# Performance work log

Measured on AMD Instinct MI355X. Metric: run time of the kernel, lower is better.

The kernel has to match this reference:

```python
import jax, jax.numpy as jnp
import numpy as np

B, C, N, H, S = 2048, 64, 64, 8, 4
D = C // H          # head dim 8
CS = C // S         # per-scale channels 16
CP = C // 4         # pattern memory dim 16


def _conv1d(x, w, b):
    # x: [B, Cin, N], w: [Cout, Cin, 3], 'same' padding
    y = jax.lax.conv_general_dilated(x, w, (1,), ((1, 1),),
                                     dimension_numbers=('NCH', 'OIH', 'NCH'))
    return y + b[None, :, None]


def setup_inputs() -> dict:
    key = jax.random.key(0)
    ks = jax.random.split(key, 20)
    s = 0.05
    f32 = jnp.float32
    return {
        'x': jax.random.normal(ks[0], (B, C, N), f32),
        'points': jax.random.normal(ks[1], (N, 3), f32),
        'conv1_w': jax.random.normal(ks[2], (S, CS, C, 3), f32) * s,
        'conv1_b': jnp.zeros((S, CS), f32),
        'conv2_w': jax.random.normal(ks[3], (S, CS, CS, 3), f32) * s,
        'conv2_b': jnp.zeros((S, CS), f32),
        'pattern_memory': jax.random.normal(ks[4], (64, CP), f32),
        'pm1_w': jax.random.normal(ks[5], (C, C + CP), f32) * s,
        'pm1_b': jnp.zeros((C,), f32),
        'pm2_w': jax.random.normal(ks[6], (C, C), f32) * s,
        'pm2_b': jnp.zeros((C,), f32),
        'q_w': jax.random.normal(ks[7], (C, C), f32) * s,
        'q_b': jnp.zeros((C,), f32),
        'k_w': jax.random.normal(ks[8], (C, C), f32) * s,
        'k_b': jnp.zeros((C,), f32),
        'v_w': jax.random.normal(ks[9], (C, C), f32) * s,
        'v_b': jnp.zeros((C,), f32),
        'in_w': jax.random.normal(ks[10], (3 * C, C), f32) * s,
        'in_b': jnp.zeros((3 * C,), f32),
        'mo_w': jax.random.normal(ks[11], (C, C), f32) * s,
        'mo_b': jnp.zeros((C,), f32),
        'out_w': jax.random.normal(ks[12], (C, C), f32) * s,
        'out_b': jnp.zeros((C,), f32),
        'ln_g': jnp.ones((C,), f32),
        'ln_beta': jnp.zeros((C,), f32),
        'adjacency': jax.random.randint(ks[13], (64, 64), 0, 2, jnp.int32),
    }


def _forward(x, points, conv1_w, conv1_b, conv2_w, conv2_b, pattern_memory,
             pm1_w, pm1_b, pm2_w, pm2_b, q_w, q_b, k_w, k_b, v_w, v_b,
             in_w, in_b, mo_w, mo_b, out_w, out_b, ln_g, ln_beta, adjacency):
    b, c, n = x.shape
    # multi-scale conv stacks (fixed small loop over scales)
    feats = []
    for i in range(S):
        y = jax.nn.relu(_conv1d(x, conv1_w[i], conv1_b[i]))
        y = jax.nn.relu(_conv1d(y, conv2_w[i], conv2_b[i]))
        feats.append(jnp.transpose(y, (0, 2, 1)))  # [B, N, CS]
    combined = jnp.concatenate(feats, axis=-1)     # [B, N, C]
    # pattern memory broadcast per point (N == 64)
    pat = jnp.broadcast_to(pattern_memory[None], (b, n, CP))
    pi = jnp.concatenate([combined, pat], axis=-1)  # [B, N, C+CP]
    pf = jax.nn.relu(pi @ pm1_w.T + pm1_b) @ pm2_w.T + pm2_b  # [B, N, C]
    q = pf @ q_w.T + q_b
    k = pf @ k_w.T + k_b
    v = pf @ v_w.T + v_b
    # nn.MultiheadAttention: internal in_proj + out_proj
    wq, wk, wv = in_w[:C], in_w[C:2 * C], in_w[2 * C:]
    bq, bk, bv = in_b[:C], in_b[C:2 * C], in_b[2 * C:]
    q2 = (q @ wq.T + bq).reshape(b, n, H, D)
    k2 = (k @ wk.T + bk).reshape(b, n, H, D)
    v2 = (v @ wv.T + bv).reshape(b, n, H, D)
    scale = 1.0 / np.sqrt(D).astype(np.float32)
    scores = jnp.einsum('bnhd,bmhd->bhnm', q2, k2) * scale
    attn = jax.nn.softmax(scores, axis=-1)
    ctx = jnp.einsum('bhnm,bmhd->bnhd', attn, v2).reshape(b, n, C)
    attended = ctx @ mo_w.T + mo_b
    # vectorized geometric bias (replaces the 64x64 python loop)
    diff = points[:, None, :] - points[None, :, :]
    dist = jnp.sqrt(jnp.sum(diff * diff, axis=-1) + 1e-12)
    geo = jnp.where(adjacency > 0, jnp.float32(0.5), -0.1 / (1.0 + dist))
    attended = attended + geo[None]
    # layer norm over channels, then output projection
    h = attended + pf
    mu = jnp.mean(h, axis=-1, keepdims=True)
    var = jnp.mean((h - mu) ** 2, axis=-1, keepdims=True)
    hn = (h - mu) * jax.lax.rsqrt(var + 1e-5) * ln_g + ln_beta
    out = hn @ out_w.T + out_b
    return jnp.transpose(out, (0, 2, 1))  # [B, C, N]


def reference(x, points, conv1_w, conv1_b, conv2_w, conv2_b, pattern_memory,
              pm1_w, pm1_b, pm2_w, pm2_b, q_w, q_b, k_w, k_b, v_w, v_b,
              in_w, in_b, mo_w, mo_b, out_w, out_b, ln_g, ln_beta, adjacency):
    return _forward(x, points, conv1_w, conv1_b, conv2_w, conv2_b,
                    pattern_memory, pm1_w, pm1_b, pm2_w, pm2_b, q_w, q_b,
                    k_w, k_b, v_w, v_b, in_w, in_b, mo_w, mo_b, out_w, out_b,
                    ln_g, ln_beta, adjacency)
```

## Files before the change

### kernel.cpp

```cpp
#include <hip/hip_runtime.h>
#include <math.h>

using bf16x8 = __attribute__((ext_vector_type(8))) __bf16;
using f32x4  = __attribute__((ext_vector_type(4))) float;

#if __has_builtin(__builtin_amdgcn_exp2f)
#define EXP2F(x) __builtin_amdgcn_exp2f(x)
#else
#define EXP2F(x) exp2f(x)
#endif

__device__ __forceinline__ unsigned short f2bf(float f) {
  unsigned u = __float_as_uint(f);
  unsigned r = u + 0x7fffu + ((u >> 16) & 1u);
  return (unsigned short)(r >> 16);
}

__device__ __forceinline__ unsigned cvt_pk_bf16(float a, float b) {
  unsigned r;
  asm("v_cvt_pk_bf16_f32 %0, %1, %2" : "=v"(r) : "v"(a), "v"(b));
  return r;
}
__device__ __forceinline__ uint2 pk4(float a, float b, float c, float d) {
  uint2 r; r.x = cvt_pk_bf16(a, b); r.y = cvt_pk_bf16(c, d); return r;
}

__device__ __forceinline__ f32x4 mfma16(uint4 a, uint4 b, f32x4 c) {
  return __builtin_amdgcn_mfma_f32_16x16x32_bf16(
      __builtin_bit_cast(bf16x8, a), __builtin_bit_cast(bf16x8, b), c, 0, 0, 0);
}
__device__ __forceinline__ float swz_xor16(float v) {
  return __int_as_float(__builtin_amdgcn_ds_swizzle(__float_as_int(v), 0x401F));
}

#define FRAG_OFF(k, n) (((((n) >> 4) * 2 + ((k) >> 5)) * 64 + (((k) >> 3) & 3) * 16 + ((n) & 15)) * 8 + ((k) & 7))

#define ATT_C 0.51006997f

__global__ void precompute_kernel(
    const float* __restrict__ conv1_w, const float* __restrict__ conv2_w,
    const float* __restrict__ pm1_w, const float* __restrict__ pm1_b,
    const float* __restrict__ pm2_w,
    const float* __restrict__ q_w, const float* __restrict__ q_b,
    const float* __restrict__ k_w, const float* __restrict__ k_b,
    const float* __restrict__ v_w, const float* __restrict__ v_b,
    const float* __restrict__ in_w, const float* __restrict__ in_b,
    const float* __restrict__ mo_w, const float* __restrict__ out_w,
    const float* __restrict__ pattern, const float* __restrict__ points,
    const int* __restrict__ adjacency,
    unsigned short* __restrict__ wsb, float* __restrict__ wsf) {
  int idx = blockIdx.x * 256 + threadIdx.x;
  if (idx < 12288) {
    int t = idx >> 12, rem = idx & 4095;
    int oc = rem >> 6, c = rem & 63;
    wsb[idx] = f2bf(conv1_w[(oc * 64 + c) * 3 + t]);
  } else if (idx < 24576) {
    int i2 = idx - 12288;
    int t = i2 >> 12, rem = i2 & 4095;
    int oc = rem >> 6, ci = rem & 63;
    float v = ((ci >> 4) == (oc >> 4)) ? conv2_w[(oc * 16 + (ci & 15)) * 3 + t] : 0.0f;
    wsb[idx] = f2bf(v);
  } else if (idx < 28672) {
    int rem = idx - 24576;
    wsb[idx] = f2bf(pm1_w[(rem >> 6) * 80 + (rem & 63)]);
  } else if (idx < 32768) {
    wsb[idx] = f2bf(pm2_w[idx - 28672]);
  } else if (idx < 36864) {
    int rem = idx - 32768; int c = rem >> 6, k = rem & 63;
    float s = 0.f;
    #pragma unroll 8
    for (int j = 0; j < 64; ++j) s += in_w[c * 64 + j] * q_w[j * 64 + k];
    wsb[idx] = f2bf(s * ATT_C);
  } else if (idx < 40960) {
    int rem = idx - 36864; int c = rem >> 6, k = rem & 63;
    float s = 0.f;
    #pragma unroll 8
    for (int j = 0; j < 64; ++j) s += in_w[(64 + c) * 64 + j] * k_w[j * 64 + k];
    wsb[idx] = f2bf(s);
  } else if (idx < 45056) {
    int rem = idx - 40960; int c = rem >> 6, k = rem & 63;
    float s = 0.f;
    #pragma unroll 8
    for (int j = 0; j < 64; ++j) s += in_w[(128 + c) * 64 + j] * v_w[j * 64 + k];
    wsb[idx] = f2bf(s);
  } else if (idx < 49152) {
    wsb[idx] = f2bf(mo_w[idx - 45056]);
  } else if (idx < 53248) {
    wsb[idx] = f2bf(out_w[idx - 49152]);
  } else if (idx < 57344) {
    int rem = idx - 53248; int c = rem >> 6, n = rem & 63;
    float s = pm1_b[c];
    #pragma unroll
    for (int cp = 0; cp < 16; ++cp) s += pm1_w[c * 80 + 64 + cp] * pattern[n * 16 + cp];
    wsf[rem] = s;
  } else if (idx < 61440) {
    int rem = idx - 57344; int c = rem >> 6, n = rem & 63;
    float dd = 1e-12f;
    #pragma unroll
    for (int i = 0; i < 3; ++i) { float d = points[n * 3 + i] - points[c * 3 + i]; dd += d * d; }
    float dist = sqrtf(dd);
    wsf[4096 + rem] = (adjacency[n * 64 + c] > 0) ? 0.5f : (-0.1f / (1.0f + dist));
  } else if (idx < 61632) {
    int rem = idx - 61440; int which = rem >> 6, c = rem & 63;
    if (which == 0) {
      float s = in_b[c];
      for (int j = 0; j < 64; ++j) s += in_w[c * 64 + j] * q_b[j];
      wsf[8192 + c] = s * ATT_C;
    } else if (which == 1) {
      float s = in_b[64 + c];
      for (int j = 0; j < 64; ++j) s += in_w[(64 + c) * 64 + j] * k_b[j];
      wsf[8256 + c] = s;
    } else {
      float s = in_b[128 + c];
      for (int j = 0; j < 64; ++j) s += in_w[(128 + c) * 64 + j] * v_b[j];
      wsf[8320 + c] = s;
    }
  }
}

__device__ __forceinline__ void gemm64(const unsigned short* __restrict__ Wg,
                                       const unsigned short* Bf,
                                       int wm, int wn, int lane, f32x4 acc[2]) {
  const int l15 = lane & 15, lq = lane >> 4;
  #pragma unroll
  for (int s = 0; s < 2; ++s) {
    bf16x8 a = *reinterpret_cast<const bf16x8*>(Wg + (16 * wm + l15) * 64 + s * 32 + lq * 8);
    #pragma unroll
    for (int nti = 0; nti < 2; ++nti) {
      int nt = 2 * wn + nti;
      bf16x8 bb = *reinterpret_cast<const bf16x8*>(Bf + ((nt * 2 + s) * 64 + lane) * 8);
      acc[nti] = __builtin_amdgcn_mfma_f32_16x16x32_bf16(a, bb, acc[nti], 0, 0, 0);
    }
  }
}

#define SLOT_B 4096
#define KBASE  8704
#define VBASE  13312
#define H32F   2048
#define LNS    6656

__global__ __launch_bounds__(512, 8) void fused_kernel(
    const float* __restrict__ x,
    const unsigned short* __restrict__ wsb, const float* __restrict__ wsf,
    const float* __restrict__ conv1_b, const float* __restrict__ conv2_b,
    const float* __restrict__ pm2_b, const float* __restrict__ mo_b,
    const float* __restrict__ out_b, const float* __restrict__ ln_g,
    const float* __restrict__ ln_beta, float* __restrict__ out) {
  __shared__ __align__(16) unsigned char smem_raw[35840];
  unsigned short* S16 = reinterpret_cast<unsigned short*>(smem_raw);
  float* S32 = reinterpret_cast<float*>(smem_raw);

  const int tid = threadIdx.x;
  const int b = blockIdx.x;
  const int lane = tid & 63;
  const int w = tid >> 6;
  const int wm = w >> 1;
  const int wn = w & 1;
  const int l15 = lane & 15;
  const int lq = lane >> 4;
  const int c0 = 16 * wm + lq * 4;
  f32x4 pfs[2];

  if (tid < 8) S16[VBASE + tid] = 0;
  {
    const float* xb = x + b * 4096 + w * 8 * 64 + lane;
    float v[8];
    #pragma unroll
    for (int j = 0; j < 8; ++j) v[j] = xb[j * 64];
    uint4 u;
    u.x = cvt_pk_bf16(v[0], v[1]);
    u.y = cvt_pk_bf16(v[2], v[3]);
    u.z = cvt_pk_bf16(v[4], v[5]);
    u.w = cvt_pk_bf16(v[6], v[7]);
    *reinterpret_cast<uint4*>(S16 + FRAG_OFF(w * 8, lane)) = u;
  }
  __syncthreads();

  auto conv_pass = [&](const unsigned short* Wg, int srcBase, f32x4 acc[2]) {
    bf16x8 a6[3][2];
    #pragma unroll
    for (int t = 0; t < 3; ++t)
      #pragma unroll
      for (int s = 0; s < 2; ++s)
        a6[t][s] = *reinterpret_cast<const bf16x8*>(Wg + t * 4096 + (16 * wm + l15) * 64 + s * 32 + lq * 8);
    #pragma unroll
    for (int nti = 0; nti < 2; ++nti) {
      int nt = 2 * wn + nti;
      #pragma unroll
      for (int t = 0; t < 3; ++t) {
        int np = nt * 16 + l15 + (t - 1);
        bool ok = (unsigned)np < 64u;
        int a = srcBase + (((np >> 4) * 2) * 64 + lq * 16 + (np & 15)) * 8;
        int A0 = ok ? a : VBASE;
        int A1 = ok ? (a + 512) : VBASE;
        bf16x8 b0 = *reinterpret_cast<const bf16x8*>(S16 + A0);
        bf16x8 b1 = *reinterpret_cast<const bf16x8*>(S16 + A1);
        acc[nti] = __builtin_amdgcn_mfma_f32_16x16x32_bf16(a6[t][0], b0, acc[nti], 0, 0, 0);
        acc[nti] = __builtin_amdgcn_mfma_f32_16x16x32_bf16(a6[t][1], b1, acc[nti], 0, 0, 0);
      }
    }
  };

  {
    f32x4 acc[2] = {};
    conv_pass(wsb, 0, acc);
    float bia[4] = {conv1_b[c0], conv1_b[c0 + 1], conv1_b[c0 + 2], conv1_b[c0 + 3]};
    #pragma unroll
    for (int nti = 0; nti < 2; ++nti) {
      int n = (2 * wn + nti) * 16 + l15;
      uint2 u = pk4(fmaxf(acc[nti][0] + bia[0], 0.f), fmaxf(acc[nti][1] + bia[1], 0.f),
                    fmaxf(acc[nti][2] + bia[2], 0.f), fmaxf(acc[nti][3] + bia[3], 0.f));
      *reinterpret_cast<uint2*>(S16 + SLOT_B + FRAG_OFF(c0, n)) = u;
    }
  }
  __syncthreads();

  {
    f32x4 acc[2] = {};
    conv_pass(wsb + 12288, SLOT_B, acc);
    float bia[4] = {conv2_b[c0], conv2_b[c0 + 1], conv2_b[c0 + 2], conv2_b[c0 + 3]};
    #pragma unroll
    for (int nti = 0; nti < 2; ++nti) {
      int n = (2 * wn + nti) * 16 + l15;
      uint2 u = pk4(fmaxf(acc[nti][0] + bia[0], 0.f), fmaxf(acc[nti][1] + bia[1], 0.f),
                    fmaxf(acc[nti][2] + bia[2], 0.f), fmaxf(acc[nti][3] + bia[3], 0.f));
      *reinterpret_cast<uint2*>(S16 + FRAG_OFF(c0, n)) = u;
    }
  }
  __syncthreads();

  {
    f32x4 acc[2] = {};
    gemm64(wsb + 24576, S16, wm, wn, lane, acc);
    #pragma unroll
    for (int nti = 0; nti < 2; ++nti) {
      int n = (2 * wn + nti) * 16 + l15;
      uint2 u = pk4(fmaxf(acc[nti][0] + wsf[(c0 + 0) * 64 + n], 0.f),
                    fmaxf(acc[nti][1] + wsf[(c0 + 1) * 64 + n], 0.f),
                    fmaxf(acc[nti][2] + wsf[(c0 + 2) * 64 + n], 0.f),
                    fmaxf(acc[nti][3] + wsf[(c0 + 3) * 64 + n], 0.f));
      *reinterpret_cast<uint2*>(S16 + SLOT_B + FRAG_OFF(c0, n)) = u;
    }
  }
  __syncthreads();

  {
    f32x4 acc[2] = {};
    gemm64(wsb + 28672, S16 + SLOT_B, wm, wn, lane, acc);
    float bia[4] = {pm2_b[c0], pm2_b[c0 + 1], pm2_b[c0 + 2], pm2_b[c0 + 3]};
    #pragma unroll
    for (int nti = 0; nti < 2; ++nti) {
      int n = (2 * wn + nti) * 16 + l15;
      f32x4 v;
      #pragma unroll
      for (int r = 0; r < 4; ++r) v[r] = acc[nti][r] + bia[r];
      pfs[nti] = v;
      *reinterpret_cast<uint2*>(S16 + FRAG_OFF(c0, n)) = pk4(v[0], v[1], v[2], v[3]);
    }
  }
  __syncthreads();

  {
    f32x4 acc[2] = {};
    gemm64(wsb + 32768, S16, wm, wn, lane, acc);
    #pragma unroll
    for (int nti = 0; nti < 2; ++nti) {
      int n = (2 * wn + nti) * 16 + l15;
      *reinterpret_cast<uint2*>(S16 + SLOT_B + n * 72 + c0) =
          pk4(acc[nti][0] + wsf[8192 + c0], acc[nti][1] + wsf[8192 + c0 + 1],
              acc[nti][2] + wsf[8192 + c0 + 2], acc[nti][3] + wsf[8192 + c0 + 3]);
    }
  }
  {
    f32x4 acc[2] = {};
    gemm64(wsb + 36864, S16, wm, wn, lane, acc);
    #pragma unroll
    for (int nti = 0; nti < 2; ++nti) {
      int n = (2 * wn + nti) * 16 + l15;
      *reinterpret_cast<uint2*>(S16 + KBASE + n * 72 + c0) =
          pk4(acc[nti][0] + wsf[8256 + c0], acc[nti][1] + wsf[8256 + c0 + 1],
              acc[nti][2] + wsf[8256 + c0 + 2], acc[nti][3] + wsf[8256 + c0 + 3]);
    }
  }
  {
    f32x4 acc[2] = {};
    gemm64(wsb + 40960, S16, wm, wn, lane, acc);
    #pragma unroll
    for (int nti = 0; nti < 2; ++nti) {
      int n = (2 * wn + nti) * 16 + l15;
      #pragma unroll
      for (int r = 0; r < 4; ++r)
        S16[VBASE + (c0 + r) * 72 + n] = f2bf(acc[nti][r] + wsf[8320 + c0 + r]);
    }
  }
  __syncthreads();

  {
    const int h = w;
    const bool lq0 = (lq == 0);
    uint4 vb[2];
    #pragma unroll
    for (int ks = 0; ks < 2; ++ks)
      vb[ks] = *reinterpret_cast<const uint4*>(
          S16 + VBASE + (h * 8 + (l15 & 7)) * 72 + ks * 32 + lq * 8);
    uint4 ka[4];
    #pragma unroll
    for (int mt = 0; mt < 4; ++mt) {
      uint4 t = *reinterpret_cast<const uint4*>(S16 + KBASE + (mt * 16 + l15) * 72 + h * 8);
      ka[mt].x = lq0 ? t.x : 0u; ka[mt].y = lq0 ? t.y : 0u;
      ka[mt].z = lq0 ? t.z : 0u; ka[mt].w = lq0 ? t.w : 0u;
    }
    __syncthreads();

    const int Pb = KBASE + w * 1152;
    #pragma unroll
    for (int q = 0; q < 4; ++q) {
      uint4 qb = *reinterpret_cast<const uint4*>(S16 + SLOT_B + (q * 16 + l15) * 72 + h * 8);
      qb.x = lq0 ? qb.x : 0u; qb.y = lq0 ? qb.y : 0u;
      qb.z = lq0 ? qb.z : 0u; qb.w = lq0 ? qb.w : 0u;
      f32x4 sc[4];
      #pragma unroll
      for (int mt = 0; mt < 4; ++mt) {
        f32x4 z = {0.f, 0.f, 0.f, 0.f};
        sc[mt] = mfma16(ka[mt], qb, z);
      }
      float sum = 0.f;
      #pragma unroll
      for (int mt = 0; mt < 4; ++mt)
        #pragma unroll
        for (int r = 0; r < 4; ++r) {
          float e = EXP2F(sc[mt][r]);
          sc[mt][r] = e; sum += e;
        }
      sum += swz_xor16(sum);
      sum += __shfl_xor(sum, 32);
      float inv = __builtin_amdgcn_rcpf(sum);
      #pragma unroll
      for (int mt = 0; mt < 4; ++mt) {
        unsigned d0 = __builtin_amdgcn_perm(__float_as_uint(sc[mt][1] * inv),
                                            __float_as_uint(sc[mt][0] * inv), 0x07060302u);
        unsigned d1 = __builtin_amdgcn_perm(__float_as_uint(sc[mt][3] * inv),
                                            __float_as_uint(sc[mt][2] * inv), 0x07060302u);
        *reinterpret_cast<uint2*>(S16 + Pb + l15 * 72 + mt * 16 + lq * 4) = make_uint2(d0, d1);
      }
      f32x4 ctx = {0.f, 0.f, 0.f, 0.f};
      #pragma unroll
      for (int ks = 0; ks < 2; ++ks) {
        uint4 pa = *reinterpret_cast<const uint4*>(S16 + Pb + l15 * 72 + ks * 32 + lq * 8);
        ctx = mfma16(pa, vb[ks], ctx);
      }
      if (l15 < 8) {
        const int kk = h * 8 + l15;
        #pragma unroll
        for (int r = 0; r < 4; ++r)
          S16[FRAG_OFF(kk, q * 16 + lq * 4 + r)] = f2bf(ctx[r]);
      }
    }
  }
  __syncthreads();

  {
    f32x4 acc[2] = {};
    gemm64(wsb + 45056, S16, wm, wn, lane, acc);
    #pragma unroll
    for (int nti = 0; nti < 2; ++nti) {
      int n = (2 * wn + nti) * 16 + l15;
      #pragma unroll
      for (int r = 0; r < 4; ++r) {
        int c = c0 + r;
        S32[H32F + c * 65 + n] = acc[nti][r] + mo_b[c] + wsf[4096 + c * 64 + n] + pfs[nti][r];
      }
    }
  }
  __syncthreads();

  {
    int n = tid & 63, qq = tid >> 6;
    float sum = 0.f, ssq = 0.f;
    #pragma unroll
    for (int j = 0; j < 8; ++j) {
      float v = S32[H32F + (qq * 8 + j) * 65 + n];
      sum += v; ssq += v * v;
    }
    S32[LNS + tid] = sum;
    S32[LNS + 512 + tid] = ssq;
    __syncthreads();
    if (tid < 64) {
      float s = 0.f, ss = 0.f;
      #pragma unroll
      for (int i = 0; i < 8; ++i) {
        s  += S32[LNS + i * 64 + tid];
        ss += S32[LNS + 512 + i * 64 + tid];
      }
      float mu = s * (1.0f / 64.0f);
      float var = ss * (1.0f / 64.0f) - mu * mu;
      S32[LNS + 1024 + tid] = mu;
      S32[LNS + 1088 + tid] = rsqrtf(var + 1e-5f);
    }
    __syncthreads();
    float mu = S32[LNS + 1024 + n], rs = S32[LNS + 1088 + n];
    int ch0 = qq * 8;
    float vv[8];
    #pragma unroll
    for (int jj = 0; jj < 8; ++jj) {
      int c = ch0 + jj;
      vv[jj] = (S32[H32F + c * 65 + n] - mu) * rs * ln_g[c] + ln_beta[c];
    }
    uint4 u;
    u.x = cvt_pk_bf16(vv[0], vv[1]);
    u.y = cvt_pk_bf16(vv[2], vv[3]);
    u.z = cvt_pk_bf16(vv[4], vv[5]);
    u.w = cvt_pk_bf16(vv[6], vv[7]);
    *reinterpret_cast<uint4*>(S16 + FRAG_OFF(ch0, n)) = u;
  }
  __syncthreads();

  {
    f32x4 acc[2] = {};
    gemm64(wsb + 49152, S16, wm, wn, lane, acc);
    float* ob = out + b * 4096;
    float bia[4] = {out_b[c0], out_b[c0 + 1], out_b[c0 + 2], out_b[c0 + 3]};
    #pragma unroll
    for (int nti = 0; nti < 2; ++nti) {
      int n = (2 * wn + nti) * 16 + l15;
      #pragma unroll
      for (int r = 0; r < 4; ++r)
        ob[(c0 + r) * 64 + n] = acc[nti][r] + bia[r];
    }
  }
}

extern "C" void kernel_launch(void* const* d_in, const int* in_sizes, int n_in,
                              void* d_out, int out_size, void* d_ws, size_t ws_size,
                              hipStream_t stream) {
  const float* x        = (const float*)d_in[0];
  const float* points   = (const float*)d_in[1];
  const float* conv1_w  = (const float*)d_in[2];
  const float* conv1_b  = (const float*)d_in[3];
  const float* conv2_w  = (const float*)d_in[4];
  const float* conv2_b  = (const float*)d_in[5];
  const float* pattern  = (const float*)d_in[6];
  const float* pm1_w    = (const float*)d_in[7];
  const float* pm1_b    = (const float*)d_in[8];
  const float* pm2_w    = (const float*)d_in[9];
  const float* pm2_b    = (const float*)d_in[10];
  const float* q_w      = (const float*)d_in[11];
  const float* q_b      = (const float*)d_in[12];
  const float* k_w      = (const float*)d_in[13];
  const float* k_b      = (const float*)d_in[14];
  const float* v_w      = (const float*)d_in[15];
  const float* v_b      = (const float*)d_in[16];
  const float* in_w     = (const float*)d_in[17];
  const float* in_b     = (const float*)d_in[18];
  const float* mo_w     = (const float*)d_in[19];
  const float* mo_b     = (const float*)d_in[20];
  const float* out_w    = (const float*)d_in[21];
  const float* out_b    = (const float*)d_in[22];
  const float* ln_g     = (const float*)d_in[23];
  const float* ln_beta  = (const float*)d_in[24];
  const int*   adjacency= (const int*)d_in[25];

  unsigned short* wsb = (unsigned short*)d_ws;
  float* wsf = (float*)((char*)d_ws + 106496);

  precompute_kernel<<<241, 256, 0, stream>>>(
      conv1_w, conv2_w, pm1_w, pm1_b, pm2_w, q_w, q_b, k_w, k_b, v_w, v_b,
      in_w, in_b, mo_w, out_w, pattern, points, adjacency, wsb, wsf);

  fused_kernel<<<2048, 512, 0, stream>>>(
      x, wsb, wsf, conv1_b, conv2_b, pm2_b, mo_b, out_b, ln_g, ln_beta,
      (float*)d_out);
}
```

Baseline: 205.9 us.

## Prefetch next-stage weights before barriers and use warp-shuffle layer norm

Loads each stage's weight fragments and biases into registers before the preceding barrier, so global latency overlaps with the wait instead of sitting on the critical path. The precomputed bias and geometry tables are reordered into the per-thread fragment layout so they load as vector reads. The V projection is computed transposed so it can be packed-stored, and softmax normalisation moves from the probabilities onto the context output. Layer norm now reduces with lane swizzles instead of shared-memory partial sums and two barriers. Launch bounds drop to 4 blocks per CU to leave room for the extra live registers, which may lower occupancy.

```diff
diff --git a/kernel.cpp b/kernel.cpp
--- a/kernel.cpp
+++ b/kernel.cpp
@@ -31,6 +31,9 @@
 }
 __device__ __forceinline__ float swz_xor16(float v) {
   return __int_as_float(__builtin_amdgcn_ds_swizzle(__float_as_int(v), 0x401F));
+}
+__device__ __forceinline__ float swz_xor8(float v) {
+  return __int_as_float(__builtin_amdgcn_ds_swizzle(__float_as_int(v), 0x201F));
 }
 
 #define FRAG_OFF(k, n) (((((n) >> 4) * 2 + ((k) >> 5)) * 64 + (((k) >> 3) & 3) * 16 + ((n) & 15)) * 8 + ((k) & 7))
@@ -88,13 +91,21 @@
   } else if (idx < 53248) {
     wsb[idx] = f2bf(out_w[idx - 49152]);
   } else if (idx < 57344) {
-    int rem = idx - 53248; int c = rem >> 6, n = rem & 63;
+    int rem = idx - 53248; int t = rem >> 3, j = rem & 7;
+    int wq = t >> 6, wm = wq >> 1, wn = wq & 1;
+    int lq = (t >> 4) & 3, l15 = t & 15;
+    int c = wm * 16 + lq * 4 + (j & 3);
+    int n = (2 * wn + (j >> 2)) * 16 + l15;
     float s = pm1_b[c];
     #pragma unroll
     for (int cp = 0; cp < 16; ++cp) s += pm1_w[c * 80 + 64 + cp] * pattern[n * 16 + cp];
     wsf[rem] = s;
   } else if (idx < 61440) {
-    int rem = idx - 57344; int c = rem >> 6, n = rem & 63;
+    int rem = idx - 57344; int t = rem >> 3, j = rem & 7;
+    int wq = t >> 6, wm = wq >> 1, wn = wq & 1;
+    int lq = (t >> 4) & 3, l15 = t & 15;
+    int c = wm * 16 + lq * 4 + (j & 3);
+    int n = (2 * wn + (j >> 2)) * 16 + l15;
     float dd = 1e-12f;
     #pragma unroll
     for (int i = 0; i < 3; ++i) { float d = points[n * 3 + i] - points[c * 3 + i]; dd += d * d; }
@@ -118,18 +129,15 @@
   }
 }
 
-__device__ __forceinline__ void gemm64(const unsigned short* __restrict__ Wg,
-                                       const unsigned short* Bf,
-                                       int wm, int wn, int lane, f32x4 acc[2]) {
-  const int l15 = lane & 15, lq = lane >> 4;
+__device__ __forceinline__ void gemm32r(const bf16x8 a[2], const unsigned short* Bf,
+                                        int wn, int lane, f32x4 acc[2]) {
   #pragma unroll
   for (int s = 0; s < 2; ++s) {
-    bf16x8 a = *reinterpret_cast<const bf16x8*>(Wg + (16 * wm + l15) * 64 + s * 32 + lq * 8);
     #pragma unroll
     for (int nti = 0; nti < 2; ++nti) {
       int nt = 2 * wn + nti;
       bf16x8 bb = *reinterpret_cast<const bf16x8*>(Bf + ((nt * 2 + s) * 64 + lane) * 8);
-      acc[nti] = __builtin_amdgcn_mfma_f32_16x16x32_bf16(a, bb, acc[nti], 0, 0, 0);
+      acc[nti] = __builtin_amdgcn_mfma_f32_16x16x32_bf16(a[s], bb, acc[nti], 0, 0, 0);
     }
   }
 }
@@ -138,9 +146,8 @@
 #define KBASE  8704
 #define VBASE  13312
 #define H32F   2048
-#define LNS    6656
-
-__global__ __launch_bounds__(512, 8) void fused_kernel(
+
+__global__ __launch_bounds__(512, 4) void fused_kernel(
     const float* __restrict__ x,
     const unsigned short* __restrict__ wsb, const float* __restrict__ wsf,
     const float* __restrict__ conv1_b, const float* __restrict__ conv2_b,
@@ -162,6 +169,16 @@
   const int c0 = 16 * wm + lq * 4;
   f32x4 pfs[2];
 
+  auto ldw = [&](int off) -> bf16x8 {
+    return *reinterpret_cast<const bf16x8*>(wsb + off + (16 * wm + l15) * 64 + lq * 8);
+  };
+
+  bf16x8 a6[3][2];
+  bf16x8 pA[2], pB[2];
+  f32x4 cp2[2], gd2[2];
+  f32x4 bq4, bk4, mo_b4, ob4;
+  float bvv[2];
+
   if (tid < 8) S16[VBASE + tid] = 0;
   {
     const float* xb = x + b * 4096 + w * 8 * 64 + lane;
@@ -175,15 +192,12 @@
     u.w = cvt_pk_bf16(v[6], v[7]);
     *reinterpret_cast<uint4*>(S16 + FRAG_OFF(w * 8, lane)) = u;
   }
-  __syncthreads();
-
-  auto conv_pass = [&](const unsigned short* Wg, int srcBase, f32x4 acc[2]) {
-    bf16x8 a6[3][2];
-    #pragma unroll
-    for (int t = 0; t < 3; ++t)
-      #pragma unroll
-      for (int s = 0; s < 2; ++s)
-        a6[t][s] = *reinterpret_cast<const bf16x8*>(Wg + t * 4096 + (16 * wm + l15) * 64 + s * 32 + lq * 8);
+  #pragma unroll
+  for (int t = 0; t < 3; ++t) { a6[t][0] = ldw(t * 4096); a6[t][1] = ldw(t * 4096 + 32); }
+  f32x4 c1b = *reinterpret_cast<const f32x4*>(conv1_b + c0);
+  __syncthreads();
+
+  auto conv_pass = [&](int srcBase, f32x4 acc[2]) {
     #pragma unroll
     for (int nti = 0; nti < 2; ++nti) {
       int nt = 2 * wn + nti;
@@ -204,94 +218,117 @@
 
   {
     f32x4 acc[2] = {};
-    conv_pass(wsb, 0, acc);
-    float bia[4] = {conv1_b[c0], conv1_b[c0 + 1], conv1_b[c0 + 2], conv1_b[c0 + 3]};
-    #pragma unroll
-    for (int nti = 0; nti < 2; ++nti) {
-      int n = (2 * wn + nti) * 16 + l15;
-      uint2 u = pk4(fmaxf(acc[nti][0] + bia[0], 0.f), fmaxf(acc[nti][1] + bia[1], 0.f),
-                    fmaxf(acc[nti][2] + bia[2], 0.f), fmaxf(acc[nti][3] + bia[3], 0.f));
+    conv_pass(0, acc);
+    #pragma unroll
+    for (int nti = 0; nti < 2; ++nti) {
+      int n = (2 * wn + nti) * 16 + l15;
+      uint2 u = pk4(fmaxf(acc[nti][0] + c1b[0], 0.f), fmaxf(acc[nti][1] + c1b[1], 0.f),
+                    fmaxf(acc[nti][2] + c1b[2], 0.f), fmaxf(acc[nti][3] + c1b[3], 0.f));
       *reinterpret_cast<uint2*>(S16 + SLOT_B + FRAG_OFF(c0, n)) = u;
     }
   }
-  __syncthreads();
-
-  {
-    f32x4 acc[2] = {};
-    conv_pass(wsb + 12288, SLOT_B, acc);
-    float bia[4] = {conv2_b[c0], conv2_b[c0 + 1], conv2_b[c0 + 2], conv2_b[c0 + 3]};
-    #pragma unroll
-    for (int nti = 0; nti < 2; ++nti) {
-      int n = (2 * wn + nti) * 16 + l15;
-      uint2 u = pk4(fmaxf(acc[nti][0] + bia[0], 0.f), fmaxf(acc[nti][1] + bia[1], 0.f),
-                    fmaxf(acc[nti][2] + bia[2], 0.f), fmaxf(acc[nti][3] + bia[3], 0.f));
+  #pragma unroll
+  for (int t = 0; t < 3; ++t) { a6[t][0] = ldw(12288 + t * 4096); a6[t][1] = ldw(12288 + t * 4096 + 32); }
+  f32x4 c2b = *reinterpret_cast<const f32x4*>(conv2_b + c0);
+  __syncthreads();
+
+  {
+    f32x4 acc[2] = {};
+    conv_pass(SLOT_B, acc);
+    #pragma unroll
+    for (int nti = 0; nti < 2; ++nti) {
+      int n = (2 * wn + nti) * 16 + l15;
+      uint2 u = pk4(fmaxf(acc[nti][0] + c2b[0], 0.f), fmaxf(acc[nti][1] + c2b[1], 0.f),
+                    fmaxf(acc[nti][2] + c2b[2], 0.f), fmaxf(acc[nti][3] + c2b[3], 0.f));
       *reinterpret_cast<uint2*>(S16 + FRAG_OFF(c0, n)) = u;
     }
   }
-  __syncthreads();
-
-  {
-    f32x4 acc[2] = {};
-    gemm64(wsb + 24576, S16, wm, wn, lane, acc);
-    #pragma unroll
-    for (int nti = 0; nti < 2; ++nti) {
-      int n = (2 * wn + nti) * 16 + l15;
-      uint2 u = pk4(fmaxf(acc[nti][0] + wsf[(c0 + 0) * 64 + n], 0.f),
-                    fmaxf(acc[nti][1] + wsf[(c0 + 1) * 64 + n], 0.f),
-                    fmaxf(acc[nti][2] + wsf[(c0 + 2) * 64 + n], 0.f),
-                    fmaxf(acc[nti][3] + wsf[(c0 + 3) * 64 + n], 0.f));
+  pA[0] = ldw(24576); pA[1] = ldw(24576 + 32);
+  cp2[0] = *reinterpret_cast<const f32x4*>(wsf + tid * 8);
+  cp2[1] = *reinterpret_cast<const f32x4*>(wsf + tid * 8 + 4);
+  __syncthreads();
+
+  {
+    f32x4 acc[2] = {};
+    gemm32r(pA, S16, wn, lane, acc);
+    #pragma unroll
+    for (int nti = 0; nti < 2; ++nti) {
+      int n = (2 * wn + nti) * 16 + l15;
+      uint2 u = pk4(fmaxf(acc[nti][0] + cp2[nti][0], 0.f),
+                    fmaxf(acc[nti][1] + cp2[nti][1], 0.f),
+                    fmaxf(acc[nti][2] + cp2[nti][2], 0.f),
+                    fmaxf(acc[nti][3] + cp2[nti][3], 0.f));
       *reinterpret_cast<uint2*>(S16 + SLOT_B + FRAG_OFF(c0, n)) = u;
     }
   }
-  __syncthreads();
-
-  {
-    f32x4 acc[2] = {};
-    gemm64(wsb + 28672, S16 + SLOT_B, wm, wn, lane, acc);
-    float bia[4] = {pm2_b[c0], pm2_b[c0 + 1], pm2_b[c0 + 2], pm2_b[c0 + 3]};
+  pA[0] = ldw(28672); pA[1] = ldw(28672 + 32);
+  f32x4 p2b = *reinterpret_cast<const f32x4*>(pm2_b + c0);
+  __syncthreads();
+
+  {
+    f32x4 acc[2] = {};
+    gemm32r(pA, S16 + SLOT_B, wn, lane, acc);
     #pragma unroll
     for (int nti = 0; nti < 2; ++nti) {
       int n = (2 * wn + nti) * 16 + l15;
       f32x4 v;
       #pragma unroll
-      for (int r = 0; r < 4; ++r) v[r] = acc[nti][r] + bia[r];
+      for (int r = 0; r < 4; ++r) v[r] = acc[nti][r] + p2b[r];
       pfs[nti] = v;
       *reinterpret_cast<uint2*>(S16 + FRAG_OFF(c0, n)) = pk4(v[0], v[1], v[2], v[3]);
     }
   }
-  __syncthreads();
-
-  {
-    f32x4 acc[2] = {};
-    gemm64(wsb + 32768, S16, wm, wn, lane, acc);
+  pA[0] = ldw(32768); pA[1] = ldw(32768 + 32);
+  pB[0] = ldw(36864); pB[1] = ldw(36864 + 32);
+  bq4 = *reinterpret_cast<const f32x4*>(wsf + 8192 + c0);
+  bk4 = *reinterpret_cast<const f32x4*>(wsf + 8256 + c0);
+  #pragma unroll
+  for (int cti = 0; cti < 2; ++cti) bvv[cti] = wsf[8320 + (2 * wn + cti) * 16 + l15];
+  __syncthreads();
+
+  {
+    f32x4 acc[2] = {};
+    gemm32r(pA, S16, wn, lane, acc);
     #pragma unroll
     for (int nti = 0; nti < 2; ++nti) {
       int n = (2 * wn + nti) * 16 + l15;
       *reinterpret_cast<uint2*>(S16 + SLOT_B + n * 72 + c0) =
-          pk4(acc[nti][0] + wsf[8192 + c0], acc[nti][1] + wsf[8192 + c0 + 1],
-              acc[nti][2] + wsf[8192 + c0 + 2], acc[nti][3] + wsf[8192 + c0 + 3]);
-    }
-  }
-  {
-    f32x4 acc[2] = {};
-    gemm64(wsb + 36864, S16, wm, wn, lane, acc);
+          pk4(acc[nti][0] + bq4[0], acc[nti][1] + bq4[1],
+              acc[nti][2] + bq4[2], acc[nti][3] + bq4[3]);
+    }
+  }
+  {
+    f32x4 acc[2] = {};
+    gemm32r(pB, S16, wn, lane, acc);
     #pragma unroll
     for (int nti = 0; nti < 2; ++nti) {
       int n = (2 * wn + nti) * 16 + l15;
       *reinterpret_cast<uint2*>(S16 + KBASE + n * 72 + c0) =
-          pk4(acc[nti][0] + wsf[8256 + c0], acc[nti][1] + wsf[8256 + c0 + 1],
-              acc[nti][2] + wsf[8256 + c0 + 2], acc[nti][3] + wsf[8256 + c0 + 3]);
-    }
-  }
-  {
-    f32x4 acc[2] = {};
-    gemm64(wsb + 40960, S16, wm, wn, lane, acc);
-    #pragma unroll
-    for (int nti = 0; nti < 2; ++nti) {
-      int n = (2 * wn + nti) * 16 + l15;
-      #pragma unroll
-      for (int r = 0; r < 4; ++r)
-        S16[VBASE + (c0 + r) * 72 + n] = f2bf(acc[nti][r] + wsf[8320 + c0 + r]);
+          pk4(acc[nti][0] + bk4[0], acc[nti][1] + bk4[1],
+              acc[nti][2] + bk4[2], acc[nti][3] + bk4[3]);
+    }
+  }
+  {
+    f32x4 acc[2] = {};
+    const unsigned short* AV = wsb + 40960;
+    #pragma unroll
+    for (int s = 0; s < 2; ++s) {
+      bf16x8 a = *reinterpret_cast<const bf16x8*>(S16 + ((wm * 2 + s) * 64 + lane) * 8);
+      #pragma unroll
+      for (int cti = 0; cti < 2; ++cti) {
+        int ct = 2 * wn + cti;
+        bf16x8 bb = *reinterpret_cast<const bf16x8*>(
+            AV + (ct * 16 + l15) * 64 + s * 32 + lq * 8);
+        acc[cti] = __builtin_amdgcn_mfma_f32_16x16x32_bf16(a, bb, acc[cti], 0, 0, 0);
+      }
+    }
+    const int m0 = 16 * wm + lq * 4;
+    #pragma unroll
+    for (int cti = 0; cti < 2; ++cti) {
+      int c = (2 * wn + cti) * 16 + l15;
+      float bia = bvv[cti];
+      *reinterpret_cast<uint2*>(S16 + VBASE + c * 72 + m0) =
+          pk4(acc[cti][0] + bia, acc[cti][1] + bia, acc[cti][2] + bia, acc[cti][3] + bia);
     }
   }
   __syncthreads();
@@ -299,12 +336,11 @@
   {
     const int h = w;
     const bool lq0 = (lq == 0);
-    uint4 vb[2];
+    uint4 vb[2], ka[4];
     #pragma unroll
     for (int ks = 0; ks < 2; ++ks)
       vb[ks] = *reinterpret_cast<const uint4*>(
           S16 + VBASE + (h * 8 + (l15 & 7)) * 72 + ks * 32 + lq * 8);
-    uint4 ka[4];
     #pragma unroll
     for (int mt = 0; mt < 4; ++mt) {
       uint4 t = *reinterpret_cast<const uint4*>(S16 + KBASE + (mt * 16 + l15) * 72 + h * 8);
@@ -317,8 +353,6 @@
     #pragma unroll
     for (int q = 0; q < 4; ++q) {
       uint4 qb = *reinterpret_cast<const uint4*>(S16 + SLOT_B + (q * 16 + l15) * 72 + h * 8);
-      qb.x = lq0 ? qb.x : 0u; qb.y = lq0 ? qb.y : 0u;
-      qb.z = lq0 ? qb.z : 0u; qb.w = lq0 ? qb.w : 0u;
       f32x4 sc[4];
       #pragma unroll
       for (int mt = 0; mt < 4; ++mt) {
@@ -333,17 +367,17 @@
           float e = EXP2F(sc[mt][r]);
           sc[mt][r] = e; sum += e;
         }
+      #pragma unroll
+      for (int mt = 0; mt < 4; ++mt) {
+        unsigned d0 = __builtin_amdgcn_perm(__float_as_uint(sc[mt][1]),
+                                            __float_as_uint(sc[mt][0]), 0x07060302u);
+        unsigned d1 = __builtin_amdgcn_perm(__float_as_uint(sc[mt][3]),
+                                            __float_as_uint(sc[mt][2]), 0x07060302u);
+        *reinterpret_cast<uint2*>(S16 + Pb + l15 * 72 + mt * 16 + lq * 4) = make_uint2(d0, d1);
+      }
       sum += swz_xor16(sum);
       sum += __shfl_xor(sum, 32);
       float inv = __builtin_amdgcn_rcpf(sum);
-      #pragma unroll
-      for (int mt = 0; mt < 4; ++mt) {
-        unsigned d0 = __builtin_amdgcn_perm(__float_as_uint(sc[mt][1] * inv),
-                                            __float_as_uint(sc[mt][0] * inv), 0x07060302u);
-        unsigned d1 = __builtin_amdgcn_perm(__float_as_uint(sc[mt][3] * inv),
-                                            __float_as_uint(sc[mt][2] * inv), 0x07060302u);
-        *reinterpret_cast<uint2*>(S16 + Pb + l15 * 72 + mt * 16 + lq * 4) = make_uint2(d0, d1);
-      }
       f32x4 ctx = {0.f, 0.f, 0.f, 0.f};
       #pragma unroll
       for (int ks = 0; ks < 2; ++ks) {
@@ -354,79 +388,76 @@
         const int kk = h * 8 + l15;
         #pragma unroll
         for (int r = 0; r < 4; ++r)
-          S16[FRAG_OFF(kk, q * 16 + lq * 4 + r)] = f2bf(ctx[r]);
-      }
-    }
-  }
-  __syncthreads();
-
-  {
-    f32x4 acc[2] = {};
-    gemm64(wsb + 45056, S16, wm, wn, lane, acc);
+          S16[FRAG_OFF(kk, q * 16 + lq * 4 + r)] = f2bf(ctx[r] * inv);
+      }
+    }
+  }
+  pA[0] = ldw(45056); pA[1] = ldw(45056 + 32);
+  mo_b4 = *reinterpret_cast<const f32x4*>(mo_b + c0);
+  gd2[0] = *reinterpret_cast<const f32x4*>(wsf + 4096 + tid * 8);
+  gd2[1] = *reinterpret_cast<const f32x4*>(wsf + 4096 + tid * 8 + 4);
+  __syncthreads();
+
+  {
+    f32x4 acc[2] = {};
+    gemm32r(pA, S16, wn, lane, acc);
     #pragma unroll
     for (int nti = 0; nti < 2; ++nti) {
       int n = (2 * wn + nti) * 16 + l15;
       #pragma unroll
       for (int r = 0; r < 4; ++r) {
         int c = c0 + r;
-        S32[H32F + c * 65 + n] = acc[nti][r] + mo_b[c] + wsf[4096 + c * 64 + n] + pfs[nti][r];
-      }
-    }
-  }
-  __syncthreads();
-
-  {
-    int n = tid & 63, qq = tid >> 6;
+        S32[H32F + c * 65 + n] = acc[nti][r] + mo_b4[r] + gd2[nti][r] + pfs[nti][r];
+      }
+    }
+  }
+  __syncthreads();
+
+  {
+    const int n8 = 8 * w + (lane & 7);
+    const int cg = lane >> 3;
+    const int ch0 = cg * 8;
+    f32x4 g0 = *reinterpret_cast<const f32x4*>(ln_g + ch0);
+    f32x4 g1 = *reinterpret_cast<const f32x4*>(ln_g + ch0 + 4);
+    f32x4 e0 = *reinterpret_cast<const f32x4*>(ln_beta + ch0);
+    f32x4 e1 = *reinterpret_cast<const f32x4*>(ln_beta + ch0 + 4);
+    float hv[8];
     float sum = 0.f, ssq = 0.f;
     #pragma unroll
     for (int j = 0; j < 8; ++j) {
-      float v = S32[H32F + (qq * 8 + j) * 65 + n];
-      sum += v; ssq += v * v;
-    }
-    S32[LNS + tid] = sum;
-    S32[LNS + 512 + tid] = ssq;
-    __syncthreads();
-    if (tid < 64) {
-      float s = 0.f, ss = 0.f;
-      #pragma unroll
-      for (int i = 0; i < 8; ++i) {
-        s  += S32[LNS + i * 64 + tid];
-        ss += S32[LNS + 512 + i * 64 + tid];
-      }
-      float mu = s * (1.0f / 64.0f);
-      float var = ss * (1.0f / 64.0f) - mu * mu;
-      S32[LNS + 1024 + tid] = mu;
-      S32[LNS + 1088 + tid] = rsqrtf(var + 1e-5f);
-    }
-    __syncthreads();
-    float mu = S32[LNS + 1024 + n], rs = S32[LNS + 1088 + n];
-    int ch0 = qq * 8;
+      float v = S32[H32F + (ch0 + j) * 65 + n8];
+      hv[j] = v; sum += v; ssq += v * v;
+    }
+    sum += swz_xor8(sum);  sum += swz_xor16(sum);  sum += __shfl_xor(sum, 32);
+    ssq += swz_xor8(ssq);  ssq += swz_xor16(ssq);  ssq += __shfl_xor(ssq, 32);
+    float mu = sum * (1.0f / 64.0f);
+    float rs = rsqrtf(ssq * (1.0f / 64.0f) - mu * mu + 1e-5f);
+    float gg[8] = {g0[0], g0[1], g0[2], g0[3], g1[0], g1[1], g1[2], g1[3]};
+    float ee[8] = {e0[0], e0[1], e0[2], e0[3], e1[0], e1[1], e1[2], e1[3]};
     float vv[8];
     #pragma unroll
-    for (int jj = 0; jj < 8; ++jj) {
-      int c = ch0 + jj;
-      vv[jj] = (S32[H32F + c * 65 + n] - mu) * rs * ln_g[c] + ln_beta[c];
-    }
+    for (int j = 0; j < 8; ++j) vv[j] = (hv[j] - mu) * rs * gg[j] + ee[j];
     uint4 u;
     u.x = cvt_pk_bf16(vv[0], vv[1]);
     u.y = cvt_pk_bf16(vv[2], vv[3]);
     u.z = cvt_pk_bf16(vv[4], vv[5]);
     u.w = cvt_pk_bf16(vv[6], vv[7]);
-    *reinterpret_cast<uint4*>(S16 + FRAG_OFF(ch0, n)) = u;
-  }
-  __syncthreads();
-
-  {
-    f32x4 acc[2] = {};
-    gemm64(wsb + 49152, S16, wm, wn, lane, acc);
+    *reinterpret_cast<uint4*>(S16 + FRAG_OFF(ch0, n8)) = u;
+  }
+  pA[0] = ldw(49152); pA[1] = ldw(49152 + 32);
+  ob4 = *reinterpret_cast<const f32x4*>(out_b + c0);
+  __syncthreads();
+
+  {
+    f32x4 acc[2] = {};
+    gemm32r(pA, S16, wn, lane, acc);
     float* ob = out + b * 4096;
-    float bia[4] = {out_b[c0], out_b[c0 + 1], out_b[c0 + 2], out_b[c0 + 3]};
     #pragma unroll
     for (int nti = 0; nti < 2; ++nti) {
       int n = (2 * wn + nti) * 16 + l15;
       #pragma unroll
       for (int r = 0; r < 4; ++r)
-        ob[(c0 + r) * 64 + n] = acc[nti][r] + bia[r];
+        ob[(c0 + r) * 64 + n] = acc[nti][r] + ob4[r];
     }
   }
 }
```

Result: faster. 191.2 us (-7.1%).
